# Kernel tuning notes

Hardware: AMD Instinct MI355X
Metric: run time of the kernel (lower is better)

The kernel has to match this reference:

```python
import jax, jax.numpy as jnp
import numpy as np
import math

N_NODES = 100000
N_EDGES = 3200000

_SQRT3 = math.sqrt(3.0)
_SQRT5 = math.sqrt(5.0)


def _spherical_harmonics_lmax2(v):
    """e3nn real spherical harmonics, lmax=2, normalize=True, normalization='component'.

    v: [E, 3] edge vectors (not necessarily unit).
    Returns [E, 9] = concat(Y0 [1], Y1 [3], Y2 [5]).
    """
    # normalize=True: evaluate SH on the unit vector
    u = v / jnp.linalg.norm(v, axis=1, keepdims=True)
    x, y, z = u[:, 0], u[:, 1], u[:, 2]
    # l=0 (component norm: *sqrt(1) = 1)
    sh0 = jnp.ones_like(x)
    # l=1 (component norm: *sqrt(3))
    sh1_0 = _SQRT3 * x
    sh1_1 = _SQRT3 * y
    sh1_2 = _SQRT3 * z
    # l=2 raw polynomials (norm-1 at unit vector), then *sqrt(5) for component norm
    x2, y2, z2 = x * x, y * y, z * z
    sh2_0 = _SQRT3 * x * z
    sh2_1 = _SQRT3 * x * y
    sh2_2 = y2 - 0.5 * (x2 + z2)
    sh2_3 = _SQRT3 * y * z
    sh2_4 = 0.5 * _SQRT3 * (z2 - x2)
    sh2 = _SQRT5 * jnp.stack([sh2_0, sh2_1, sh2_2, sh2_3, sh2_4], axis=-1)
    return jnp.concatenate(
        [sh0[:, None], jnp.stack([sh1_0, sh1_1, sh1_2], axis=-1), sh2], axis=-1
    )


def setup_inputs() -> dict:
    key = jax.random.key(0)
    k1, k2, k3 = jax.random.split(key, 3)
    pos = jax.random.normal(k1, (N_NODES, 3), dtype=jnp.float32)
    edge_index = jax.random.randint(k2, (2, N_EDGES), 0, N_NODES, dtype=jnp.int64)
    shift = jax.random.normal(k3, (N_EDGES, 3), dtype=jnp.float32)
    return {"pos": pos, "edge_index": edge_index, "shift": shift}


def reference(pos, edge_index, shift):
    # gather endpoints and form displacement vectors
    edge_vec = pos[edge_index[1]] - pos[edge_index[0]]  # [E, 3]
    edge_vec = edge_vec - shift
    edge_length = jnp.linalg.norm(edge_vec, axis=1)  # [E]
    edge_sh = _spherical_harmonics_lmax2(edge_vec)  # [E, 9]
    return (edge_vec, edge_length, edge_sh)
```

## Files before the change

### kernel.cpp

```cpp
#include <hip/hip_runtime.h>
#include <math.h>


#define SQRT3 1.7320508075688772f
#define SQRT5 2.2360679774997896f

__global__ __launch_bounds__(256) void sh_edge_kernel(
    const float*  __restrict__ pos,
    const int*    __restrict__ edge_index,
    const float*  __restrict__ shift,
    float* __restrict__ out_vec,
    float* __restrict__ out_len,
    float* __restrict__ out_sh,
    int n_edges)
{
    const int e = blockIdx.x * 256 + threadIdx.x;
    if (e >= n_edges) return;

    const int s = __builtin_nontemporal_load(&edge_index[e]);
    const int d = __builtin_nontemporal_load(&edge_index[n_edges + e]);

    const float* sp = shift + 3 * (size_t)e;
    const float shx = sp[0], shy = sp[1], shz = sp[2];

    const float* ps = pos + 3 * (size_t)s;
    const float* pd = pos + 3 * (size_t)d;
    const float ax = ps[0], ay = ps[1], az = ps[2];
    const float bx = pd[0], by = pd[1], bz = pd[2];

    const float x = bx - ax - shx;
    const float y = by - ay - shy;
    const float z = bz - az - shz;

    {
        float* ov = out_vec + 3 * (size_t)e;
        __builtin_nontemporal_store(x, &ov[0]);
        __builtin_nontemporal_store(y, &ov[1]);
        __builtin_nontemporal_store(z, &ov[2]);
    }

    const float sq = x * x + y * y + z * z;
    const float r  = rsqrtf(sq);
    __builtin_nontemporal_store(sq * r, &out_len[e]);

    const float nx = x * r, ny = y * r, nz = z * r;
    const float x2 = nx * nx, y2 = ny * ny, z2 = nz * nz;

    float* o = out_sh + 9 * (size_t)e;
    o[0] = 1.0f;
    o[1] = SQRT3 * nx;
    o[2] = SQRT3 * ny;
    o[3] = SQRT3 * nz;
    o[4] = SQRT5 * SQRT3 * nx * nz;
    o[5] = SQRT5 * SQRT3 * nx * ny;
    o[6] = SQRT5 * (y2 - 0.5f * (x2 + z2));
    o[7] = SQRT5 * SQRT3 * ny * nz;
    o[8] = SQRT5 * 0.5f * SQRT3 * (z2 - x2);
}

extern "C" void kernel_launch(void* const* d_in, const int* in_sizes, int n_in,
                              void* d_out, int out_size, void* d_ws, size_t ws_size,
                              hipStream_t stream) {
    const float* pos        = (const float*)d_in[0];
    const int*   edge_index = (const int*)d_in[1];
    const float* shift      = (const float*)d_in[2];

    const int n_edges = in_sizes[2] / 3;

    float* out_vec = (float*)d_out;
    float* out_len = (float*)d_out + 3 * (size_t)n_edges;
    float* out_sh  = (float*)d_out + 4 * (size_t)n_edges;

    const int blocks = (n_edges + 255) / 256;
    sh_edge_kernel<<<blocks, 256, 0, stream>>>(
        pos, edge_index, shift, out_vec, out_len, out_sh, n_edges);
}
```

Before: 271.4 us.

## Convert to grid-stride loop with software-pipelined index and position prefetch

```diff
diff --git a/kernel.cpp b/kernel.cpp
--- a/kernel.cpp
+++ b/kernel.cpp
@@ -14,48 +14,89 @@
     float* __restrict__ out_sh,
     int n_edges)
 {
-    const int e = blockIdx.x * 256 + threadIdx.x;
-    if (e >= n_edges) return;
+    const int stride = gridDim.x * 256;
 
-    const int s = __builtin_nontemporal_load(&edge_index[e]);
-    const int d = __builtin_nontemporal_load(&edge_index[n_edges + e]);
-
-    const float* sp = shift + 3 * (size_t)e;
-    const float shx = sp[0], shy = sp[1], shz = sp[2];
-
-    const float* ps = pos + 3 * (size_t)s;
-    const float* pd = pos + 3 * (size_t)d;
-    const float ax = ps[0], ay = ps[1], az = ps[2];
-    const float bx = pd[0], by = pd[1], bz = pd[2];
-
-    const float x = bx - ax - shx;
-    const float y = by - ay - shy;
-    const float z = bz - az - shz;
-
-    {
-        float* ov = out_vec + 3 * (size_t)e;
-        __builtin_nontemporal_store(x, &ov[0]);
-        __builtin_nontemporal_store(y, &ov[1]);
-        __builtin_nontemporal_store(z, &ov[2]);
+    int  e1 = blockIdx.x * 256 + threadIdx.x;
+    bool a1 = e1 < n_edges;
+    int  s1 = 0, d1 = 0;
+    if (a1) {
+        s1 = __builtin_nontemporal_load(&edge_index[e1]);
+        d1 = __builtin_nontemporal_load(&edge_index[n_edges + e1]);
+    }
+    float ax1=0.f, ay1=0.f, az1=0.f, bx1=0.f, by1=0.f, bz1=0.f;
+    float hx1=0.f, hy1=0.f, hz1=0.f;
+    if (a1) {
+        const float* ps = pos + 3 * (size_t)s1;
+        const float* pd = pos + 3 * (size_t)d1;
+        ax1 = ps[0]; ay1 = ps[1]; az1 = ps[2];
+        bx1 = pd[0]; by1 = pd[1]; bz1 = pd[2];
+        const float* sp = shift + 3 * (size_t)e1;
+        hx1 = __builtin_nontemporal_load(&sp[0]);
+        hy1 = __builtin_nontemporal_load(&sp[1]);
+        hz1 = __builtin_nontemporal_load(&sp[2]);
+    }
+    int  e2 = e1 + stride;
+    bool a2 = e2 < n_edges;
+    int  s2 = 0, d2 = 0;
+    if (a2) {
+        s2 = __builtin_nontemporal_load(&edge_index[e2]);
+        d2 = __builtin_nontemporal_load(&edge_index[n_edges + e2]);
     }
 
-    const float sq = x * x + y * y + z * z;
-    const float r  = rsqrtf(sq);
-    __builtin_nontemporal_store(sq * r, &out_len[e]);
+    while (a1) {
+        {
+            const float x = bx1 - ax1 - hx1;
+            const float y = by1 - ay1 - hy1;
+            const float z = bz1 - az1 - hz1;
+            float* ov = out_vec + 3 * (size_t)e1;
+            __builtin_nontemporal_store(x, &ov[0]);
+            __builtin_nontemporal_store(y, &ov[1]);
+            __builtin_nontemporal_store(z, &ov[2]);
+            const float sq = x * x + y * y + z * z;
+            const float r  = rsqrtf(sq);
+            __builtin_nontemporal_store(sq * r, &out_len[e1]);
+            const float nx = x * r, ny = y * r, nz = z * r;
+            const float x2 = nx * nx, y2 = ny * ny, z2 = nz * nz;
+            float* o = out_sh + 9 * (size_t)e1;
+            __builtin_nontemporal_store(1.0f,                          &o[0]);
+            __builtin_nontemporal_store(SQRT3 * nx,                    &o[1]);
+            __builtin_nontemporal_store(SQRT3 * ny,                    &o[2]);
+            __builtin_nontemporal_store(SQRT3 * nz,                    &o[3]);
+            __builtin_nontemporal_store(SQRT5 * SQRT3 * nx * nz,       &o[4]);
+            __builtin_nontemporal_store(SQRT5 * SQRT3 * nx * ny,       &o[5]);
+            __builtin_nontemporal_store(SQRT5 * (y2 - 0.5f*(x2 + z2)), &o[6]);
+            __builtin_nontemporal_store(SQRT5 * SQRT3 * ny * nz,       &o[7]);
+            __builtin_nontemporal_store(SQRT5 * 0.5f * SQRT3 * (z2 - x2), &o[8]);
+        }
 
-    const float nx = x * r, ny = y * r, nz = z * r;
-    const float x2 = nx * nx, y2 = ny * ny, z2 = nz * nz;
+        if (!a2) break;
 
-    float* o = out_sh + 9 * (size_t)e;
-    o[0] = 1.0f;
-    o[1] = SQRT3 * nx;
-    o[2] = SQRT3 * ny;
-    o[3] = SQRT3 * nz;
-    o[4] = SQRT5 * SQRT3 * nx * nz;
-    o[5] = SQRT5 * SQRT3 * nx * ny;
-    o[6] = SQRT5 * (y2 - 0.5f * (x2 + z2));
-    o[7] = SQRT5 * SQRT3 * ny * nz;
-    o[8] = SQRT5 * 0.5f * SQRT3 * (z2 - x2);
+        float ax2, ay2, az2, bx2, by2, bz2, hx2, hy2, hz2;
+        {
+            const float* ps = pos + 3 * (size_t)s2;
+            const float* pd = pos + 3 * (size_t)d2;
+            ax2 = ps[0]; ay2 = ps[1]; az2 = ps[2];
+            bx2 = pd[0]; by2 = pd[1]; bz2 = pd[2];
+            const float* sp = shift + 3 * (size_t)e2;
+            hx2 = __builtin_nontemporal_load(&sp[0]);
+            hy2 = __builtin_nontemporal_load(&sp[1]);
+            hz2 = __builtin_nontemporal_load(&sp[2]);
+        }
+
+        const int  e3 = e2 + stride;
+        const bool a3 = e3 < n_edges;
+        int s3 = 0, d3 = 0;
+        if (a3) {
+            s3 = __builtin_nontemporal_load(&edge_index[e3]);
+            d3 = __builtin_nontemporal_load(&edge_index[n_edges + e3]);
+        }
+
+        e1 = e2; a1 = a2;
+        ax1 = ax2; ay1 = ay2; az1 = az2;
+        bx1 = bx2; by1 = by2; bz1 = bz2;
+        hx1 = hx2; hy1 = hy2; hz1 = hz2;
+        e2 = e3; a2 = a3; s2 = s3; d2 = d3;
+    }
 }
 
 extern "C" void kernel_launch(void* const* d_in, const int* in_sizes, int n_in,
@@ -71,7 +112,8 @@
     float* out_len = (float*)d_out + 3 * (size_t)n_edges;
     float* out_sh  = (float*)d_out + 4 * (size_t)n_edges;
 
-    const int blocks = (n_edges + 255) / 256;
+    int blocks = (n_edges + 255) / 256;
+    if (blocks > 2048) blocks = 2048;
     sh_edge_kernel<<<blocks, 256, 0, stream>>>(
         pos, edge_index, shift, out_vec, out_len, out_sh, n_edges);
 }
```

Result: no change. 272.3 us (+0.3%).

## Use persistent grid with software-pipelined gathers and LDS-staged SH stores

Applied to the files above, without the earlier changes.

```diff
diff --git a/kernel.cpp b/kernel.cpp
--- a/kernel.cpp
+++ b/kernel.cpp
@@ -4,6 +4,11 @@
 
 #define SQRT3 1.7320508075688772f
 #define SQRT5 2.2360679774997896f
+
+typedef float v4f __attribute__((ext_vector_type(4)));
+
+#define NTL(p)    __builtin_nontemporal_load(p)
+#define NTS(v, p) __builtin_nontemporal_store((v), (p))
 
 __global__ __launch_bounds__(256) void sh_edge_kernel(
     const float*  __restrict__ pos,
@@ -14,48 +19,134 @@
     float* __restrict__ out_sh,
     int n_edges)
 {
-    const int e = blockIdx.x * 256 + threadIdx.x;
-    if (e >= n_edges) return;
+    __shared__ float s_sh[4608];
+    const int tid     = threadIdx.x;
+    const int n_tiles = (n_edges + 511) >> 9;
+    const int tstride = gridDim.x;
 
-    const int s = __builtin_nontemporal_load(&edge_index[e]);
-    const int d = __builtin_nontemporal_load(&edge_index[n_edges + e]);
+    int t_cur = blockIdx.x;
+    if (t_cur >= n_tiles) return;
 
-    const float* sp = shift + 3 * (size_t)e;
-    const float shx = sp[0], shy = sp[1], shz = sp[2];
-
-    const float* ps = pos + 3 * (size_t)s;
-    const float* pd = pos + 3 * (size_t)d;
-    const float ax = ps[0], ay = ps[1], az = ps[2];
-    const float bx = pd[0], by = pd[1], bz = pd[2];
-
-    const float x = bx - ax - shx;
-    const float y = by - ay - shy;
-    const float z = bz - az - shz;
+    float aAx=0,aAy=0,aAz=0,bAx=0,bAy=0,bAz=0,hAx=0,hAy=0,hAz=0;
+    float aBx=0,aBy=0,aBz=0,bBx=0,bBy=0,bBz=0,hBx=0,hBy=0,hBz=0;
+    int nAs=0,nAd=0,nBs=0,nBd=0;
 
     {
-        float* ov = out_vec + 3 * (size_t)e;
-        __builtin_nontemporal_store(x, &ov[0]);
-        __builtin_nontemporal_store(y, &ov[1]);
-        __builtin_nontemporal_store(z, &ov[2]);
+        const int base = t_cur << 9;
+        const int eA = base + tid, eB = eA + 256;
+        int sA=0,dA=0,sB=0,dB=0;
+        const bool vA = eA < n_edges, vB = eB < n_edges;
+        if (vA) { sA = NTL(&edge_index[eA]); dA = NTL(&edge_index[n_edges + eA]); }
+        if (vB) { sB = NTL(&edge_index[eB]); dB = NTL(&edge_index[n_edges + eB]); }
+        if (vA) {
+            const float* p = pos + 3 * (size_t)sA; aAx=p[0]; aAy=p[1]; aAz=p[2];
+            const float* q = pos + 3 * (size_t)dA; bAx=q[0]; bAy=q[1]; bAz=q[2];
+            const float* sp = shift + 3 * (size_t)eA;
+            hAx=NTL(&sp[0]); hAy=NTL(&sp[1]); hAz=NTL(&sp[2]);
+        }
+        if (vB) {
+            const float* p = pos + 3 * (size_t)sB; aBx=p[0]; aBy=p[1]; aBz=p[2];
+            const float* q = pos + 3 * (size_t)dB; bBx=q[0]; bBy=q[1]; bBz=q[2];
+            const float* sp = shift + 3 * (size_t)eB;
+            hBx=NTL(&sp[0]); hBy=NTL(&sp[1]); hBz=NTL(&sp[2]);
+        }
+    }
+    int t_nxt = t_cur + tstride;
+    if (t_nxt < n_tiles) {
+        const int base = t_nxt << 9;
+        const int eA = base + tid, eB = eA + 256;
+        if (eA < n_edges) { nAs = NTL(&edge_index[eA]); nAd = NTL(&edge_index[n_edges + eA]); }
+        if (eB < n_edges) { nBs = NTL(&edge_index[eB]); nBd = NTL(&edge_index[n_edges + eB]); }
     }
 
-    const float sq = x * x + y * y + z * z;
-    const float r  = rsqrtf(sq);
-    __builtin_nontemporal_store(sq * r, &out_len[e]);
+    while (true) {
+        const int  base      = t_cur << 9;
+        const bool have_next = (t_nxt < n_tiles);
 
-    const float nx = x * r, ny = y * r, nz = z * r;
-    const float x2 = nx * nx, y2 = ny * ny, z2 = nz * nz;
+        float xaAx=0,xaAy=0,xaAz=0,xbAx=0,xbAy=0,xbAz=0,xhAx=0,xhAy=0,xhAz=0;
+        float xaBx=0,xaBy=0,xaBz=0,xbBx=0,xbBy=0,xbBz=0,xhBx=0,xhBy=0,xhBz=0;
+        if (have_next) {
+            const int nb = t_nxt << 9;
+            const int eA = nb + tid, eB = eA + 256;
+            if (eA < n_edges) {
+                const float* p = pos + 3 * (size_t)nAs; xaAx=p[0]; xaAy=p[1]; xaAz=p[2];
+                const float* q = pos + 3 * (size_t)nAd; xbAx=q[0]; xbAy=q[1]; xbAz=q[2];
+                const float* sp = shift + 3 * (size_t)eA;
+                xhAx=NTL(&sp[0]); xhAy=NTL(&sp[1]); xhAz=NTL(&sp[2]);
+            }
+            if (eB < n_edges) {
+                const float* p = pos + 3 * (size_t)nBs; xaBx=p[0]; xaBy=p[1]; xaBz=p[2];
+                const float* q = pos + 3 * (size_t)nBd; xbBx=q[0]; xbBy=q[1]; xbBz=q[2];
+                const float* sp = shift + 3 * (size_t)eB;
+                xhBx=NTL(&sp[0]); xhBy=NTL(&sp[1]); xhBz=NTL(&sp[2]);
+            }
+        }
 
-    float* o = out_sh + 9 * (size_t)e;
-    o[0] = 1.0f;
-    o[1] = SQRT3 * nx;
-    o[2] = SQRT3 * ny;
-    o[3] = SQRT3 * nz;
-    o[4] = SQRT5 * SQRT3 * nx * nz;
-    o[5] = SQRT5 * SQRT3 * nx * ny;
-    o[6] = SQRT5 * (y2 - 0.5f * (x2 + z2));
-    o[7] = SQRT5 * SQRT3 * ny * nz;
-    o[8] = SQRT5 * 0.5f * SQRT3 * (z2 - x2);
+        const int t_n2 = t_nxt + tstride;
+        int mAs=0,mAd=0,mBs=0,mBd=0;
+        if (t_n2 < n_tiles) {
+            const int nb = t_n2 << 9;
+            const int eA = nb + tid, eB = eA + 256;
+            if (eA < n_edges) { mAs = NTL(&edge_index[eA]); mAd = NTL(&edge_index[n_edges + eA]); }
+            if (eB < n_edges) { mBs = NTL(&edge_index[eB]); mBd = NTL(&edge_index[n_edges + eB]); }
+        }
+
+        const int nblk = min(512, n_edges - base);
+#define EDGE_COMPUTE(k, AX,AY,AZ, BX,BY,BZ, HX,HY,HZ)                     \
+        {                                                                 \
+            const int e = base + (k);                                     \
+            const float x = (BX) - (AX) - (HX);                           \
+            const float y = (BY) - (AY) - (HY);                           \
+            const float z = (BZ) - (AZ) - (HZ);                           \
+            float* ov = out_vec + 3 * (size_t)e;                          \
+            NTS(x, &ov[0]); NTS(y, &ov[1]); NTS(z, &ov[2]);               \
+            const float sq = x*x + y*y + z*z;                             \
+            const float r  = rsqrtf(sq);                                  \
+            NTS(sq * r, &out_len[e]);                                     \
+            const float nx = x*r, ny = y*r, nz = z*r;                     \
+            const float x2 = nx*nx, y2 = ny*ny, z2 = nz*nz;               \
+            float* o = s_sh + 9 * (k);                                    \
+            o[0] = 1.0f;                                                  \
+            o[1] = SQRT3 * nx;                                            \
+            o[2] = SQRT3 * ny;                                            \
+            o[3] = SQRT3 * nz;                                            \
+            o[4] = SQRT5 * SQRT3 * nx * nz;                               \
+            o[5] = SQRT5 * SQRT3 * nx * ny;                               \
+            o[6] = SQRT5 * (y2 - 0.5f * (x2 + z2));                       \
+            o[7] = SQRT5 * SQRT3 * ny * nz;                               \
+            o[8] = SQRT5 * 0.5f * SQRT3 * (z2 - x2);                      \
+        }
+        if (tid < nblk)
+            EDGE_COMPUTE(tid,       aAx,aAy,aAz, bAx,bAy,bAz, hAx,hAy,hAz);
+        if (tid + 256 < nblk)
+            EDGE_COMPUTE(tid + 256, aBx,aBy,aBz, bBx,bBy,bBz, hBx,hBy,hBz);
+#undef EDGE_COMPUTE
+        __syncthreads();
+
+        if (nblk == 512) {
+            v4f* gs = reinterpret_cast<v4f*>(out_sh + 9 * (size_t)base);
+            const v4f* ls = reinterpret_cast<const v4f*>(s_sh);
+            NTS(ls[tid],        &gs[tid]);
+            NTS(ls[tid + 256],  &gs[tid + 256]);
+            NTS(ls[tid + 512],  &gs[tid + 512]);
+            NTS(ls[tid + 768],  &gs[tid + 768]);
+            if (tid < 128)
+                NTS(ls[tid + 1024], &gs[tid + 1024]);
+        } else {
+            for (int i = tid; i < 9 * nblk; i += 256)
+                out_sh[9 * (size_t)base + i] = s_sh[i];
+        }
+
+        if (!have_next) break;
+        __syncthreads();
+
+        t_cur = t_nxt; t_nxt = t_n2;
+        aAx=xaAx; aAy=xaAy; aAz=xaAz; bAx=xbAx; bAy=xbAy; bAz=xbAz;
+        hAx=xhAx; hAy=xhAy; hAz=xhAz;
+        aBx=xaBx; aBy=xaBy; aBz=xaBz; bBx=xbBx; bBy=xbBy; bBz=xbBz;
+        hBx=xhBx; hBy=xhBy; hBz=xhBz;
+        nAs=mAs; nAd=mAd; nBs=mBs; nBd=mBd;
+    }
 }
 
 extern "C" void kernel_launch(void* const* d_in, const int* in_sizes, int n_in,
@@ -71,7 +162,8 @@
     float* out_len = (float*)d_out + 3 * (size_t)n_edges;
     float* out_sh  = (float*)d_out + 4 * (size_t)n_edges;
 
-    const int blocks = (n_edges + 255) / 256;
+    const int n_tiles = (n_edges + 511) / 512;
+    int blocks = n_tiles < 2048 ? n_tiles : 2048;
     sh_edge_kernel<<<blocks, 256, 0, stream>>>(
         pos, edge_index, shift, out_vec, out_len, out_sh, n_edges);
 }
```

Result: faster. 253.5 us (-6.6%).

## Pipeline gathers across grid-stride chunks and stage outputs in LDS for vector stores

Applied to the files above, without the earlier changes.

```diff
diff --git a/kernel.cpp b/kernel.cpp
--- a/kernel.cpp
+++ b/kernel.cpp
@@ -4,6 +4,11 @@
 
 #define SQRT3 1.7320508075688772f
 #define SQRT5 2.2360679774997896f
+
+typedef float v4f __attribute__((ext_vector_type(4)));
+
+#define NTL(p)    __builtin_nontemporal_load(p)
+#define NTS(v, p) __builtin_nontemporal_store((v), (p))
 
 __global__ __launch_bounds__(256) void sh_edge_kernel(
     const float*  __restrict__ pos,
@@ -14,48 +19,125 @@
     float* __restrict__ out_sh,
     int n_edges)
 {
-    const int e = blockIdx.x * 256 + threadIdx.x;
-    if (e >= n_edges) return;
+    __shared__ float s_buf[4][768];
 
-    const int s = __builtin_nontemporal_load(&edge_index[e]);
-    const int d = __builtin_nontemporal_load(&edge_index[n_edges + e]);
+    const int lane = threadIdx.x & 63;
+    const int wid  = threadIdx.x >> 6;
+    float* s_vec = s_buf[wid];
+    float* s_sh  = s_buf[wid] + 192;
 
-    const float* sp = shift + 3 * (size_t)e;
-    const float shx = sp[0], shy = sp[1], shz = sp[2];
+    const int n_chunks = (n_edges + 63) >> 6;
+    const int wstride  = gridDim.x << 2;
 
-    const float* ps = pos + 3 * (size_t)s;
-    const float* pd = pos + 3 * (size_t)d;
-    const float ax = ps[0], ay = ps[1], az = ps[2];
-    const float bx = pd[0], by = pd[1], bz = pd[2];
+    int c1 = (blockIdx.x << 2) + wid;
+    if (c1 >= n_chunks) return;
 
-    const float x = bx - ax - shx;
-    const float y = by - ay - shy;
-    const float z = bz - az - shz;
-
+    int  e1 = (c1 << 6) + lane;
+    bool v1 = e1 < n_edges;
+    float ax1=0,ay1=0,az1=0,bx1=0,by1=0,bz1=0,hx1=0,hy1=0,hz1=0;
     {
-        float* ov = out_vec + 3 * (size_t)e;
-        __builtin_nontemporal_store(x, &ov[0]);
-        __builtin_nontemporal_store(y, &ov[1]);
-        __builtin_nontemporal_store(z, &ov[2]);
+        int s=0,d=0;
+        if (v1) { s = NTL(&edge_index[e1]); d = NTL(&edge_index[n_edges + e1]); }
+        if (v1) {
+            const float* p = pos + 3 * (size_t)s; ax1=p[0]; ay1=p[1]; az1=p[2];
+            const float* q = pos + 3 * (size_t)d; bx1=q[0]; by1=q[1]; bz1=q[2];
+            const float* sp = shift + 3 * (size_t)e1;
+            hx1=NTL(&sp[0]); hy1=NTL(&sp[1]); hz1=NTL(&sp[2]);
+        }
+    }
+    int  c2 = c1 + wstride;
+    int  s2 = 0, d2 = 0;
+    bool v2 = false;
+    if (c2 < n_chunks) {
+        const int e2 = (c2 << 6) + lane;
+        v2 = e2 < n_edges;
+        if (v2) { s2 = NTL(&edge_index[e2]); d2 = NTL(&edge_index[n_edges + e2]); }
     }
 
-    const float sq = x * x + y * y + z * z;
-    const float r  = rsqrtf(sq);
-    __builtin_nontemporal_store(sq * r, &out_len[e]);
+    while (true) {
+        const bool have_next = (c2 < n_chunks);
 
-    const float nx = x * r, ny = y * r, nz = z * r;
-    const float x2 = nx * nx, y2 = ny * ny, z2 = nz * nz;
+        float xax=0,xay=0,xaz=0,xbx=0,xby=0,xbz=0,xhx=0,xhy=0,xhz=0;
+        if (have_next && v2) {
+            const int e2 = (c2 << 6) + lane;
+            const float* p = pos + 3 * (size_t)s2; xax=p[0]; xay=p[1]; xaz=p[2];
+            const float* q = pos + 3 * (size_t)d2; xbx=q[0]; xby=q[1]; xbz=q[2];
+            const float* sp = shift + 3 * (size_t)e2;
+            xhx=NTL(&sp[0]); xhy=NTL(&sp[1]); xhz=NTL(&sp[2]);
+        }
 
-    float* o = out_sh + 9 * (size_t)e;
-    o[0] = 1.0f;
-    o[1] = SQRT3 * nx;
-    o[2] = SQRT3 * ny;
-    o[3] = SQRT3 * nz;
-    o[4] = SQRT5 * SQRT3 * nx * nz;
-    o[5] = SQRT5 * SQRT3 * nx * ny;
-    o[6] = SQRT5 * (y2 - 0.5f * (x2 + z2));
-    o[7] = SQRT5 * SQRT3 * ny * nz;
-    o[8] = SQRT5 * 0.5f * SQRT3 * (z2 - x2);
+        const int c3 = c2 + wstride;
+        int s3=0, d3=0; bool v3=false;
+        if (c3 < n_chunks) {
+            const int e3 = (c3 << 6) + lane;
+            v3 = e3 < n_edges;
+            if (v3) { s3 = NTL(&edge_index[e3]); d3 = NTL(&edge_index[n_edges + e3]); }
+        }
+
+        const int base = c1 << 6;
+        const bool full = (base + 64 <= n_edges);
+        if (full) {
+            const float x = bx1 - ax1 - hx1;
+            const float y = by1 - ay1 - hy1;
+            const float z = bz1 - az1 - hz1;
+            s_vec[3*lane + 0] = x;
+            s_vec[3*lane + 1] = y;
+            s_vec[3*lane + 2] = z;
+            const float sq = x*x + y*y + z*z;
+            const float r  = rsqrtf(sq);
+            NTS(sq * r, &out_len[e1]);
+            const float nx = x*r, ny = y*r, nz = z*r;
+            const float x2 = nx*nx, y2 = ny*ny, z2 = nz*nz;
+            float* o = s_sh + 9*lane;
+            o[0] = 1.0f;
+            o[1] = SQRT3 * nx;
+            o[2] = SQRT3 * ny;
+            o[3] = SQRT3 * nz;
+            o[4] = SQRT5 * SQRT3 * nx * nz;
+            o[5] = SQRT5 * SQRT3 * nx * ny;
+            o[6] = SQRT5 * (y2 - 0.5f * (x2 + z2));
+            o[7] = SQRT5 * SQRT3 * ny * nz;
+            o[8] = SQRT5 * 0.5f * SQRT3 * (z2 - x2);
+
+            v4f* gv = reinterpret_cast<v4f*>(out_vec + 3 * (size_t)base);
+            const v4f* lv = reinterpret_cast<const v4f*>(s_vec);
+            if (lane < 48) NTS(lv[lane], &gv[lane]);
+
+            v4f* gs = reinterpret_cast<v4f*>(out_sh + 9 * (size_t)base);
+            const v4f* ls = reinterpret_cast<const v4f*>(s_sh);
+            NTS(ls[lane],      &gs[lane]);
+            NTS(ls[lane + 64], &gs[lane + 64]);
+            if (lane < 16) NTS(ls[lane + 128], &gs[lane + 128]);
+        } else if (v1) {
+            const float x = bx1 - ax1 - hx1;
+            const float y = by1 - ay1 - hy1;
+            const float z = bz1 - az1 - hz1;
+            float* ov = out_vec + 3 * (size_t)e1;
+            ov[0] = x; ov[1] = y; ov[2] = z;
+            const float sq = x*x + y*y + z*z;
+            const float r  = rsqrtf(sq);
+            out_len[e1] = sq * r;
+            const float nx = x*r, ny = y*r, nz = z*r;
+            const float x2 = nx*nx, y2 = ny*ny, z2 = nz*nz;
+            float* o = out_sh + 9 * (size_t)e1;
+            o[0] = 1.0f;
+            o[1] = SQRT3 * nx;
+            o[2] = SQRT3 * ny;
+            o[3] = SQRT3 * nz;
+            o[4] = SQRT5 * SQRT3 * nx * nz;
+            o[5] = SQRT5 * SQRT3 * nx * ny;
+            o[6] = SQRT5 * (y2 - 0.5f * (x2 + z2));
+            o[7] = SQRT5 * SQRT3 * ny * nz;
+            o[8] = SQRT5 * 0.5f * SQRT3 * (z2 - x2);
+        }
+
+        if (!have_next) break;
+
+        c1 = c2; e1 = (c1 << 6) + lane; v1 = v2;
+        ax1=xax; ay1=xay; az1=xaz; bx1=xbx; by1=xby; bz1=xbz;
+        hx1=xhx; hy1=xhy; hz1=xhz;
+        c2 = c3; s2 = s3; d2 = d3; v2 = v3;
+    }
 }
 
 extern "C" void kernel_launch(void* const* d_in, const int* in_sizes, int n_in,
@@ -71,7 +153,9 @@
     float* out_len = (float*)d_out + 3 * (size_t)n_edges;
     float* out_sh  = (float*)d_out + 4 * (size_t)n_edges;
 
-    const int blocks = (n_edges + 255) / 256;
+    const int n_chunks = (n_edges + 63) / 64;
+    int blocks = (n_chunks + 3) / 4;
+    if (blocks > 2048) blocks = 2048;
     sh_edge_kernel<<<blocks, 256, 0, stream>>>(
         pos, edge_index, shift, out_vec, out_len, out_sh, n_edges);
 }
```

After: 258.6 us. 1.05x faster.
